# Kernel tuning notes

Measured on AMD Instinct MI355X. Metric: run time of the kernel, lower is better.

## Reference

```python
import jax, jax.numpy as jnp
import numpy as np

N = 4096
D_FEAT = 64


def setup_inputs() -> dict:
    key = jax.random.key(0)
    kx, ky = jax.random.split(key)
    xINP = jax.random.normal(kx, (N, D_FEAT), dtype=jnp.float32)
    yINP = jax.random.normal(ky, (N, D_FEAT), dtype=jnp.float32)
    return {"xINP": xINP, "yINP": yINP}


def _greedy_match(xINP, yINP):
    n = xINP.shape[0]
    # Euclidean (p=2) distance matrix, same as scipy.spatial.distance_matrix
    x2 = jnp.sum(xINP * xINP, axis=1)[:, None]           # [n, 1]
    y2 = jnp.sum(yINP * yINP, axis=1)[None, :]           # [1, n]
    sq = jnp.maximum(x2 + y2 - 2.0 * (xINP @ yINP.T), 0.0)
    cost = jnp.sqrt(sq)                                   # [n, n]
    # sorted() with key is stable; jnp.argsort is stable by default
    order = jnp.argsort(cost.reshape(-1))                 # [n*n]

    row0 = jnp.full((n,), -1, dtype=jnp.int32)
    col0 = jnp.full((n,), -1, dtype=jnp.int32)

    def body(k, state):
        row, col = state
        idx = order[k]
        i = idx // n
        j = idx % n
        free = (row[i] == -1) & (col[j] == -1)
        row = row.at[i].set(jnp.where(free, j.astype(jnp.int32), row[i]))
        col = col.at[j].set(jnp.where(free, i.astype(jnp.int32), col[j]))
        return (row, col)

    row, _col = jax.lax.fori_loop(0, n * n, body, (row0, col0))
    return row  # row_to_col_match_vec, int32 in [-1, n)


def reference(xINP, yINP):
    return _greedy_match(xINP, yINP)
```

## Files before the change

### kernel.cpp

```cpp
#include <hip/hip_runtime.h>

#define N 4096
#define D 64
#define TCAP 1024
#define TTHRESH 96
#define SNB 256
#define SNT 512
#define S0B 1024
#define S0T 512
#define RPAIRS 14

typedef unsigned long long u64;

__device__ float g_C[(size_t)N * (size_t)N];
__device__ float g_tailC[(size_t)TCAP * TCAP];
__device__ float4 g_yT[N * 16];
__device__ float g_x2[N], g_y2[N];
__device__ int   g_rowMatch[N];
__device__ int   g_freeRows[2][N];
__device__ int   g_freeCols[2][N];
__device__ u64   g_rowMinR[2][N];
__device__ u64   g_colMin[2][N];
__device__ int   g_nr[2], g_nc[2];
__device__ int   g_done, g_finalCur;

__device__ inline u64 shfl_down_u64(u64 v, int d) {
  unsigned lo = (unsigned)(v & 0xffffffffull);
  unsigned hi = (unsigned)(v >> 32);
  lo = __shfl_down(lo, d, 64);
  hi = __shfl_down(hi, d, 64);
  return ((u64)hi << 32) | (u64)lo;
}

__device__ inline void block_rowmin_reduce8(u64* best, int rows, u64* s_part) {
  const int tid = threadIdx.x;
  const int lane = tid & 63;
  const int wv = tid >> 6;
#pragma unroll
  for (int r = 0; r < 16; ++r) {
    if (r < rows) {
      u64 v = best[r];
#pragma unroll
      for (int d = 32; d > 0; d >>= 1) {
        u64 o = shfl_down_u64(v, d);
        v = (o < v) ? o : v;
      }
      if (lane == 0) s_part[r * 8 + wv] = v;
    }
  }
  __syncthreads();
  if (tid < rows) {
    u64 mn = s_part[tid * 8];
#pragma unroll
    for (int w = 1; w < 8; ++w) {
      u64 o = s_part[tid * 8 + w];
      mn = (o < mn) ? o : mn;
    }
    s_part[128 + tid] = mn;
  }
}

__device__ __forceinline__ float f4e(const float4* a, int e) {
  float4 v = a[e >> 2];
  switch (e & 3) {
    case 0: return v.x;
    case 1: return v.y;
    case 2: return v.z;
    default: return v.w;
  }
}

__global__ void __launch_bounds__(256) k_init(const float* __restrict__ x,
                                              const float* __restrict__ y) {
  const int i = blockIdx.x * 256 + threadIdx.x;
  const float4* xr4 = reinterpret_cast<const float4*>(x + (size_t)i * D);
  const float4* yr4 = reinterpret_cast<const float4*>(y + (size_t)i * D);

  {
    float4 xv[16];
#pragma unroll
    for (int k = 0; k < 16; ++k) xv[k] = xr4[k];
    float qx[8];
#pragma unroll
    for (int j = 0; j < 8; ++j) {
      float v = f4e(xv, j);
      qx[j] = __fmul_rn(v, v);
    }
#pragma unroll
    for (int m = 8; m < D; m += 8) {
#pragma unroll
      for (int j = 0; j < 8; ++j) {
        float v = f4e(xv, m + j);
        qx[j] = __fadd_rn(qx[j], __fmul_rn(v, v));
      }
    }
    g_x2[i] = __fadd_rn(__fadd_rn(__fadd_rn(qx[0], qx[1]), __fadd_rn(qx[2], qx[3])),
                        __fadd_rn(__fadd_rn(qx[4], qx[5]), __fadd_rn(qx[6], qx[7])));
  }
  {
    float4 yv[16];
#pragma unroll
    for (int k = 0; k < 16; ++k) yv[k] = yr4[k];
    float qy[8];
#pragma unroll
    for (int j = 0; j < 8; ++j) {
      float w = f4e(yv, j);
      qy[j] = __fmul_rn(w, w);
    }
#pragma unroll
    for (int m = 8; m < D; m += 8) {
#pragma unroll
      for (int j = 0; j < 8; ++j) {
        float w = f4e(yv, m + j);
        qy[j] = __fadd_rn(qy[j], __fmul_rn(w, w));
      }
    }
    g_y2[i] = __fadd_rn(__fadd_rn(__fadd_rn(qy[0], qy[1]), __fadd_rn(qy[2], qy[3])),
                        __fadd_rn(__fadd_rn(qy[4], qy[5]), __fadd_rn(qy[6], qy[7])));
#pragma unroll
    for (int k = 0; k < 16; ++k) g_yT[(k << 12) + i] = yv[k];
  }

  g_rowMatch[i] = -1;
  g_freeRows[0][i] = i;
  g_freeCols[0][i] = i;
  g_rowMinR[0][i] = ~0ull;
  g_rowMinR[1][i] = ~0ull;
  g_colMin[0][i] = ~0ull;
  g_colMin[1][i] = ~0ull;
  if (i == 0) {
    g_nr[0] = N; g_nc[0] = N; g_nr[1] = 0; g_nc[1] = 0;
    g_done = 0;
    g_finalCur = ((RPAIRS & 1) ^ 1);
  }
}

__global__ void __launch_bounds__(S0T) k_scan0(const float* __restrict__ x,
                                               const float* __restrict__ y) {
  __shared__ u64 s_part[64 + 8];
  const int tid = threadIdx.x;
  const int r0 = (blockIdx.x >> 1) << 3;
  const int h = blockIdx.x & 1;

  float x2r[8];
#pragma unroll
  for (int r = 0; r < 8; ++r) x2r[r] = g_x2[r0 + r];
  u64 best[8];
#pragma unroll
  for (int r = 0; r < 8; ++r) best[r] = ~0ull;

  const int c0 = tid + (h << 11);
  float acc[8][4];
#pragma unroll
  for (int r = 0; r < 8; ++r)
#pragma unroll
    for (int k = 0; k < 4; ++k) acc[r][k] = 0.0f;

#pragma unroll
  for (int kc = 0; kc < 16; ++kc) {
    const float4* ytk = g_yT + (kc << 12);
    float4 yv0 = ytk[c0];
    float4 yv1 = ytk[c0 + 512];
    float4 yv2 = ytk[c0 + 1024];
    float4 yv3 = ytk[c0 + 1536];
#pragma unroll
    for (int r = 0; r < 8; ++r) {
      float4 xv = reinterpret_cast<const float4*>(x + (size_t)(r0 + r) * D)[kc];
      acc[r][0] = fmaf(xv.x, yv0.x, acc[r][0]);
      acc[r][0] = fmaf(xv.y, yv0.y, acc[r][0]);
      acc[r][0] = fmaf(xv.z, yv0.z, acc[r][0]);
      acc[r][0] = fmaf(xv.w, yv0.w, acc[r][0]);
      acc[r][1] = fmaf(xv.x, yv1.x, acc[r][1]);
      acc[r][1] = fmaf(xv.y, yv1.y, acc[r][1]);
      acc[r][1] = fmaf(xv.z, yv1.z, acc[r][1]);
      acc[r][1] = fmaf(xv.w, yv1.w, acc[r][1]);
      acc[r][2] = fmaf(xv.x, yv2.x, acc[r][2]);
      acc[r][2] = fmaf(xv.y, yv2.y, acc[r][2]);
      acc[r][2] = fmaf(xv.z, yv2.z, acc[r][2]);
      acc[r][2] = fmaf(xv.w, yv2.w, acc[r][2]);
      acc[r][3] = fmaf(xv.x, yv3.x, acc[r][3]);
      acc[r][3] = fmaf(xv.y, yv3.y, acc[r][3]);
      acc[r][3] = fmaf(xv.z, yv3.z, acc[r][3]);
      acc[r][3] = fmaf(xv.w, yv3.w, acc[r][3]);
    }
  }

#pragma unroll
  for (int k = 0; k < 4; ++k) {
    const int c = c0 + (k << 9);
    const float y2j = g_y2[c];
    u64 ckey = ~0ull;
#pragma unroll
    for (int r = 0; r < 8; ++r) {
      float t = __fadd_rn(x2r[r], y2j);
      float sq = __fsub_rn(t, __fmul_rn(2.0f, acc[r][k]));
      sq = fmaxf(sq, 0.0f);
      float cost = __fsqrt_rn(sq);
      g_C[(size_t)(r0 + r) * N + c] = cost;
      u64 cb = ((u64)__float_as_uint(cost)) << 32;
      u64 rk = cb | (unsigned)c;
      best[r] = (rk < best[r]) ? rk : best[r];
      u64 ck = cb | (unsigned)(r0 + r);
      ckey = (ck < ckey) ? ck : ckey;
    }
    u64 curv = g_colMin[0][c];
    if (ckey < curv) atomicMin((unsigned long long*)&g_colMin[0][c], ckey);
  }

  {
    const int lane = tid & 63, wv = tid >> 6;
#pragma unroll
    for (int r = 0; r < 8; ++r) {
      u64 v = best[r];
#pragma unroll
      for (int d = 32; d > 0; d >>= 1) {
        u64 o = shfl_down_u64(v, d);
        v = (o < v) ? o : v;
      }
      if (lane == 0) s_part[r * 8 + wv] = v;
    }
    __syncthreads();
    if (tid < 8) {
      u64 mn = s_part[tid * 8];
#pragma unroll
      for (int w = 1; w < 8; ++w) {
        u64 o = s_part[tid * 8 + w];
        mn = (o < mn) ? o : mn;
      }
      u64 curv = g_rowMinR[0][r0 + tid];
      if (mn < curv) atomicMin((unsigned long long*)&g_rowMinR[0][r0 + tid], mn);
    }
  }
  (void)y;
}

__global__ void __launch_bounds__(SNT, 2) k_scanN(int round) {
  if (g_done) return;
  const int cur = round & 1;
  const int nr = g_nr[cur], nc = g_nc[cur];
  const int tid = threadIdx.x, bid = blockIdx.x;

  for (int t = bid * SNT + tid; t < N; t += SNB * SNT) {
    g_colMin[cur ^ 1][t] = ~0ull;
    g_rowMinR[cur ^ 1][t] = ~0ull;
  }

  const int ngroups = (nr + 15) >> 4;
  int lgS = 0;
  while (lgS < 4 && (ngroups << (lgS + 1)) <= SNB) ++lgS;
  const int S = 1 << lgS;
  if (bid >= (ngroups << lgS)) return;
  const int g = bid >> lgS;
  const int s = bid & (S - 1);

  __shared__ u64 s_colPart[4096];
  __shared__ u64 s_part[128 + 16];
  __shared__ int s_irow[16];

  const int r0 = g << 4;
  const int rows = min(16, nr - r0);
  if (tid < 16) {
    int rr = (tid < rows) ? (r0 + tid) : r0;
    s_irow[tid] = g_freeRows[cur][rr];
  }
  const int cstart = (s << 9) + tid;
  const int cstep = S << 9;
  for (int c = cstart; c < nc; c += cstep) s_colPart[c] = ~0ull;
  __syncthreads();

  int ir[16];
#pragma unroll
  for (int r = 0; r < 16; ++r) ir[r] = s_irow[r];
  u64 best[16];
#pragma unroll
  for (int r = 0; r < 16; ++r) best[r] = ~0ull;

  for (int c = cstart; c < nc; c += cstep) {
    const int j = g_freeCols[cur][c];
    u64 cpart = s_colPart[c];
#pragma unroll
    for (int r = 0; r < 16; ++r) {
      if (r < rows) {
        float cost = g_C[(size_t)ir[r] * N + j];
        u64 cb = ((u64)__float_as_uint(cost)) << 32;
        u64 rk = cb | (unsigned)j;
        best[r] = (rk < best[r]) ? rk : best[r];
        u64 ck = cb | (unsigned)ir[r];
        cpart = (ck < cpart) ? ck : cpart;
      }
    }
    s_colPart[c] = cpart;
  }

  block_rowmin_reduce8(best, rows, s_part);
  if (tid < rows) {
    u64 k = s_part[128 + tid];
    u64 curv = g_rowMinR[cur][s_irow[tid]];
    if (k < curv) atomicMin((unsigned long long*)&g_rowMinR[cur][s_irow[tid]], k);
  }

  for (int c = cstart; c < nc; c += cstep) {
    u64 k = s_colPart[c];
    if (k != ~0ull) {
      int j = g_freeCols[cur][c];
      u64 curv = g_colMin[cur][j];
      if (k < curv) atomicMin((unsigned long long*)&g_colMin[cur][j], k);
    }
  }
}

__global__ void __launch_bounds__(SNT) k_match(int round) {
  if (g_done) return;
  const int cur = round & 1, nxt = cur ^ 1;
  const int tid = threadIdx.x, bid = blockIdx.x;
  const int nr = g_nr[cur], nc = g_nc[cur];
  __shared__ int s_wc[8];
  __shared__ int s_base;

  const int lane = tid & 63, wv = tid >> 6;
  if (bid == 0) {
    if (tid == 0) s_base = 0;
    __syncthreads();
    for (int start = 0; start < nr; start += SNT) {
      int r = start + tid;
      int keep = 0; int iv = -1;
      if (r < nr) {
        int i = g_freeRows[cur][r];
        iv = i;
        int j = (int)(unsigned)(g_rowMinR[cur][i] & 0xffffffffull);
        u64 cm = g_colMin[cur][j];
        if ((int)(unsigned)(cm & 0xffffffffull) == i) g_rowMatch[i] = j;
        else keep = 1;
      }
      u64 bm = __ballot(keep);
      int pre = __popcll(bm & ((1ull << lane) - 1ull));
      if (lane == 0) s_wc[wv] = __popcll(bm);
      __syncthreads();
      int off = 0, tot = 0;
#pragma unroll
      for (int w = 0; w < 8; ++w) { off += (w < wv) ? s_wc[w] : 0; tot += s_wc[w]; }
      if (keep) g_freeRows[nxt][s_base + off + pre] = iv;
      __syncthreads();
      if (tid == 0) s_base += tot;
      __syncthreads();
    }
    if (tid == 0) {
      int nnr = s_base;
      g_nr[nxt] = nnr;
      if (nnr <= TTHRESH || nnr >= nr) { g_finalCur = nxt; g_done = 1; }
    }
  } else {
    if (tid == 0) s_base = 0;
    __syncthreads();
    for (int start = 0; start < nc; start += SNT) {
      int c = start + tid;
      int keep = 0; int jv = -1;
      if (c < nc) {
        int j = g_freeCols[cur][c];
        jv = j;
        u64 cm = g_colMin[cur][j];
        int i2 = (int)(unsigned)(cm & 0xffffffffull);
        int bj = (int)(unsigned)(g_rowMinR[cur][i2] & 0xffffffffull);
        if (bj != j) keep = 1;
      }
      u64 bm = __ballot(keep);
      int pre = __popcll(bm & ((1ull << lane) - 1ull));
      if (lane == 0) s_wc[wv] = __popcll(bm);
      __syncthreads();
      int off = 0, tot = 0;
#pragma unroll
      for (int w = 0; w < 8; ++w) { off += (w < wv) ? s_wc[w] : 0; tot += s_wc[w]; }
      if (keep) g_freeCols[nxt][s_base + off + pre] = jv;
      __syncthreads();
      if (tid == 0) s_base += tot;
      __syncthreads();
    }
    if (tid == 0) g_nc[nxt] = s_base;
  }
}

__global__ void __launch_bounds__(SNT) k_gather() {
  const int fc = g_finalCur;
  const int mr = g_nr[fc], mc = g_nc[fc];
  if (mr <= 0 || mr > TCAP || mc <= 0 || mc > TCAP) return;
  const int tid = threadIdx.x, bid = blockIdx.x;
  for (int rr = bid; rr < mr; rr += SNB) {
    const int irow = g_freeRows[fc][rr];
    const float* src = g_C + (size_t)irow * N;
    float* dst = g_tailC + (size_t)rr * TCAP;
    for (int c = tid; c < mc; c += SNT) {
      dst[c] = src[g_freeCols[fc][c]];
    }
  }
}

__global__ void __launch_bounds__(1024, 1) k_tail(int* __restrict__ out) {
  __shared__ int s_rpos[2][TCAP], s_cpos[2][TCAP];
  __shared__ int s_rbest[TCAP];
  __shared__ u64 s_cmin[TCAP];
  __shared__ int s_wc[16];
  const int tid = threadIdx.x;
  const int lane = tid & 63, wv = tid >> 6;

  const int fc = g_finalCur;
  int mr = g_nr[fc], mc = g_nc[fc];
  if (mr < 0 || mr > TCAP || mc < 0 || mc > TCAP) mr = 0;
  for (int t = tid; t < mr; t += 1024) s_rpos[0][t] = t;
  for (int t = tid; t < mc; t += 1024) s_cpos[0][t] = t;
  __syncthreads();

  int tcur = 0;
  for (int round = 0; round < 2048 && mr > 0; ++round) {
    const int nit = (mc + 63) >> 6;
    int cpv[16];
#pragma unroll
    for (int k = 0; k < 16; ++k) {
      int ci = (k << 6) + lane;
      cpv[k] = (k < nit && ci < mc) ? s_cpos[tcur][ci] : 0;
    }
    for (int rr = wv; rr < mr; rr += 16) {
      const int rp = s_rpos[tcur][rr];
      const float* rowp = g_tailC + (size_t)rp * TCAP;
      u64 best = ~0ull;
#pragma unroll
      for (int k = 0; k < 16; ++k) {
        if (k < nit) {
          int ci = (k << 6) + lane;
          if (ci < mc) {
            float cost = rowp[cpv[k]];
            u64 key = (((u64)__float_as_uint(cost)) << 32) | (unsigned)ci;
            best = (key < best) ? key : best;
          }
        }
      }
#pragma unroll
      for (int d = 32; d > 0; d >>= 1) {
        u64 o = shfl_down_u64(best, d);
        best = (o < best) ? o : best;
      }
      if (lane == 0) s_rbest[rr] = (int)(best & 0xffffffffull);
    }
    __syncthreads();
    if (tid < mc) {
      const int cp = s_cpos[tcur][tid];
      const float* colp = g_tailC + cp;
      u64 best = ~0ull;
      int r = 0;
      for (; r + 4 <= mr; r += 4) {
#pragma unroll
        for (int q = 0; q < 4; ++q) {
          int rp = s_rpos[tcur][r + q];
          float cost = colp[(size_t)rp * TCAP];
          u64 key = (((u64)__float_as_uint(cost)) << 32) | (unsigned)(r + q);
          best = (key < best) ? key : best;
        }
      }
      for (; r < mr; ++r) {
        int rp = s_rpos[tcur][r];
        float cost = colp[(size_t)rp * TCAP];
        u64 key = (((u64)__float_as_uint(cost)) << 32) | (unsigned)r;
        best = (key < best) ? key : best;
      }
      s_cmin[tid] = best;
    }
    __syncthreads();
    int keep = 0;
    if (tid < mr) {
      int q = s_rbest[tid];
      if ((int)(unsigned)(s_cmin[q] & 0xffffffffull) == tid) {
        g_rowMatch[g_freeRows[fc][s_rpos[tcur][tid]]] = g_freeCols[fc][s_cpos[tcur][q]];
      } else keep = 1;
    }
    u64 bm = __ballot(keep);
    int pre = __popcll(bm & ((1ull << lane) - 1ull));
    if (lane == 0) s_wc[wv] = __popcll(bm);
    __syncthreads();
    int off = 0, tot = 0;
#pragma unroll
    for (int w = 0; w < 16; ++w) { off += (w < wv) ? s_wc[w] : 0; tot += s_wc[w]; }
    if (keep) s_rpos[tcur ^ 1][off + pre] = s_rpos[tcur][tid];
    int newmr = tot;
    __syncthreads();
    int keepc = 0;
    if (tid < mc) {
      int r2 = (int)(unsigned)(s_cmin[tid] & 0xffffffffull);
      if (s_rbest[r2] != tid) keepc = 1;
    }
    u64 bm2 = __ballot(keepc);
    int pre2 = __popcll(bm2 & ((1ull << lane) - 1ull));
    if (lane == 0) s_wc[wv] = __popcll(bm2);
    __syncthreads();
    int off2 = 0, tot2 = 0;
#pragma unroll
    for (int w = 0; w < 16; ++w) { off2 += (w < wv) ? s_wc[w] : 0; tot2 += s_wc[w]; }
    if (keepc) s_cpos[tcur ^ 1][off2 + pre2] = s_cpos[tcur][tid];
    __syncthreads();
    if (newmr >= mr) break;
    mr = newmr; mc = tot2; tcur ^= 1;
  }
  __syncthreads();
  for (int i = tid; i < N; i += 1024) out[i] = g_rowMatch[i];
}

extern "C" void kernel_launch(void* const* d_in, const int* in_sizes, int n_in,
                              void* d_out, int out_size, void* d_ws, size_t ws_size,
                              hipStream_t stream) {
  const float* x = (const float*)d_in[0];
  const float* y = (const float*)d_in[1];
  int* out = (int*)d_out;
  k_init<<<16, 256, 0, stream>>>(x, y);
  k_scan0<<<S0B, S0T, 0, stream>>>(x, y);
  k_match<<<2, SNT, 0, stream>>>(0);
  for (int r = 1; r <= RPAIRS; ++r) {
    k_scanN<<<SNB, SNT, 0, stream>>>(r);
    k_match<<<2, SNT, 0, stream>>>(r);
  }
  k_gather<<<SNB, SNT, 0, stream>>>();
  k_tail<<<1, 1024, 0, stream>>>(out);
  (void)in_sizes; (void)n_in; (void)out_size; (void)d_ws; (void)ws_size;
}
```

Before: 787.7 us.

## Track top-2 row/col minima to match more pairs per round

The scan kernel now keeps the two smallest keys per free row and per free column, and merges them with paired atomicMin inserts. The match kernel uses these second minima to resolve a second tier of mutual-best pairs: a pair whose first choice was taken by another mutual match can still be committed in the same round. The aim is to shrink the free set faster so fewer scan/match rounds are needed, and RPAIRS drops from 14 to 9 to match. In exchange each scan pass costs more (extra shared memory, registers, compares and atomics), and the second-tier logic may not exactly reproduce the greedy order.

```diff
diff --git a/kernel.cpp b/kernel.cpp
--- a/kernel.cpp
+++ b/kernel.cpp
@@ -8,9 +8,10 @@
 #define SNT 512
 #define S0B 1024
 #define S0T 512
-#define RPAIRS 14
+#define RPAIRS 9
 
 typedef unsigned long long u64;
+#define LO32(k) ((int)(unsigned)((k) & 0xffffffffull))
 
 __device__ float g_C[(size_t)N * (size_t)N];
 __device__ float g_tailC[(size_t)TCAP * TCAP];
@@ -20,7 +21,9 @@
 __device__ int   g_freeRows[2][N];
 __device__ int   g_freeCols[2][N];
 __device__ u64   g_rowMinR[2][N];
+__device__ u64   g_rowMin2[2][N];
 __device__ u64   g_colMin[2][N];
+__device__ u64   g_colMin2[2][N];
 __device__ int   g_nr[2], g_nc[2];
 __device__ int   g_done, g_finalCur;
 
@@ -70,6 +73,13 @@
   }
 }
 
+__device__ __forceinline__ void insert2(u64* m1, u64* m2, u64 k) {
+  if (k == ~0ull) return;
+  u64 old = atomicMin((unsigned long long*)m1, k);
+  u64 loser = (k < old) ? old : k;
+  if (loser != ~0ull) atomicMin((unsigned long long*)m2, loser);
+}
+
 __global__ void __launch_bounds__(256) k_init(const float* __restrict__ x,
                                               const float* __restrict__ y) {
   const int i = blockIdx.x * 256 + threadIdx.x;
@@ -126,8 +136,12 @@
   g_freeCols[0][i] = i;
   g_rowMinR[0][i] = ~0ull;
   g_rowMinR[1][i] = ~0ull;
+  g_rowMin2[0][i] = ~0ull;
+  g_rowMin2[1][i] = ~0ull;
   g_colMin[0][i] = ~0ull;
   g_colMin[1][i] = ~0ull;
+  g_colMin2[0][i] = ~0ull;
+  g_colMin2[1][i] = ~0ull;
   if (i == 0) {
     g_nr[0] = N; g_nc[0] = N; g_nr[1] = 0; g_nc[1] = 0;
     g_done = 0;
@@ -242,7 +256,9 @@
 
   for (int t = bid * SNT + tid; t < N; t += SNB * SNT) {
     g_colMin[cur ^ 1][t] = ~0ull;
+    g_colMin2[cur ^ 1][t] = ~0ull;
     g_rowMinR[cur ^ 1][t] = ~0ull;
+    g_rowMin2[cur ^ 1][t] = ~0ull;
   }
 
   const int ngroups = (nr + 15) >> 4;
@@ -253,8 +269,10 @@
   const int g = bid >> lgS;
   const int s = bid & (S - 1);
 
-  __shared__ u64 s_colPart[4096];
-  __shared__ u64 s_part[128 + 16];
+  __shared__ u64 s_cp1[4096];
+  __shared__ u64 s_cp2[4096];
+  __shared__ u64 s_p1[128 + 16];
+  __shared__ u64 s_p2[128 + 16];
   __shared__ int s_irow[16];
 
   const int r0 = g << 4;
@@ -265,46 +283,78 @@
   }
   const int cstart = (s << 9) + tid;
   const int cstep = S << 9;
-  for (int c = cstart; c < nc; c += cstep) s_colPart[c] = ~0ull;
+  for (int c = cstart; c < nc; c += cstep) { s_cp1[c] = ~0ull; s_cp2[c] = ~0ull; }
   __syncthreads();
 
   int ir[16];
 #pragma unroll
   for (int r = 0; r < 16; ++r) ir[r] = s_irow[r];
-  u64 best[16];
-#pragma unroll
-  for (int r = 0; r < 16; ++r) best[r] = ~0ull;
+  u64 b1[16], b2[16];
+#pragma unroll
+  for (int r = 0; r < 16; ++r) { b1[r] = ~0ull; b2[r] = ~0ull; }
 
   for (int c = cstart; c < nc; c += cstep) {
     const int j = g_freeCols[cur][c];
-    u64 cpart = s_colPart[c];
+    u64 c1 = s_cp1[c], c2 = s_cp2[c];
 #pragma unroll
     for (int r = 0; r < 16; ++r) {
       if (r < rows) {
         float cost = g_C[(size_t)ir[r] * N + j];
         u64 cb = ((u64)__float_as_uint(cost)) << 32;
         u64 rk = cb | (unsigned)j;
-        best[r] = (rk < best[r]) ? rk : best[r];
+        if (rk < b1[r]) { b2[r] = b1[r]; b1[r] = rk; }
+        else if (rk < b2[r]) b2[r] = rk;
         u64 ck = cb | (unsigned)ir[r];
-        cpart = (ck < cpart) ? ck : cpart;
-      }
-    }
-    s_colPart[c] = cpart;
-  }
-
-  block_rowmin_reduce8(best, rows, s_part);
-  if (tid < rows) {
-    u64 k = s_part[128 + tid];
-    u64 curv = g_rowMinR[cur][s_irow[tid]];
-    if (k < curv) atomicMin((unsigned long long*)&g_rowMinR[cur][s_irow[tid]], k);
+        if (ck < c1) { c2 = c1; c1 = ck; }
+        else if (ck < c2) c2 = ck;
+      }
+    }
+    s_cp1[c] = c1; s_cp2[c] = c2;
+  }
+
+  {
+    const int lane = tid & 63, wv = tid >> 6;
+#pragma unroll
+    for (int r = 0; r < 16; ++r) {
+      if (r < rows) {
+        u64 v1 = b1[r], v2 = b2[r];
+#pragma unroll
+        for (int d = 32; d > 0; d >>= 1) {
+          u64 o1 = shfl_down_u64(v1, d);
+          u64 o2 = shfl_down_u64(v2, d);
+          u64 n1 = (v1 < o1) ? v1 : o1;
+          u64 hi = (v1 < o1) ? o1 : v1;
+          u64 lo = (v2 < o2) ? v2 : o2;
+          v1 = n1;
+          v2 = (hi < lo) ? hi : lo;
+        }
+        if (lane == 0) { s_p1[r * 8 + wv] = v1; s_p2[r * 8 + wv] = v2; }
+      }
+    }
+    __syncthreads();
+    if (tid < rows) {
+      u64 m1 = s_p1[tid * 8], m2 = s_p2[tid * 8];
+#pragma unroll
+      for (int w = 1; w < 8; ++w) {
+        u64 o1 = s_p1[tid * 8 + w], o2 = s_p2[tid * 8 + w];
+        u64 n1 = (m1 < o1) ? m1 : o1;
+        u64 hi = (m1 < o1) ? o1 : m1;
+        u64 lo = (m2 < o2) ? m2 : o2;
+        m1 = n1;
+        m2 = (hi < lo) ? hi : lo;
+      }
+      const int i = s_irow[tid];
+      insert2(&g_rowMinR[cur][i], &g_rowMin2[cur][i], m1);
+      insert2(&g_rowMinR[cur][i], &g_rowMin2[cur][i], m2);
+    }
   }
 
   for (int c = cstart; c < nc; c += cstep) {
-    u64 k = s_colPart[c];
-    if (k != ~0ull) {
-      int j = g_freeCols[cur][c];
-      u64 curv = g_colMin[cur][j];
-      if (k < curv) atomicMin((unsigned long long*)&g_colMin[cur][j], k);
+    u64 k1 = s_cp1[c];
+    if (k1 != ~0ull) {
+      const int j = g_freeCols[cur][c];
+      insert2(&g_colMin[cur][j], &g_colMin2[cur][j], k1);
+      insert2(&g_colMin[cur][j], &g_colMin2[cur][j], s_cp2[c]);
     }
   }
 }
@@ -327,10 +377,41 @@
       if (r < nr) {
         int i = g_freeRows[cur][r];
         iv = i;
-        int j = (int)(unsigned)(g_rowMinR[cur][i] & 0xffffffffull);
-        u64 cm = g_colMin[cur][j];
-        if ((int)(unsigned)(cm & 0xffffffffull) == i) g_rowMatch[i] = j;
-        else keep = 1;
+        u64 rm1 = g_rowMinR[cur][i];
+        int j1 = LO32(rm1);
+        int i1 = LO32(g_colMin[cur][j1]);
+        if (i1 == i) {
+          g_rowMatch[i] = j1;
+        } else {
+          int jc = -1;
+          bool j1gone = (LO32(g_rowMinR[cur][i1]) == j1);
+          if (!j1gone) jc = j1;
+          else {
+            u64 rm2 = g_rowMin2[cur][i];
+            if (rm2 != ~0ull) {
+              int j2 = LO32(rm2);
+              int i2 = LO32(g_colMin[cur][j2]);
+              if (LO32(g_rowMinR[cur][i2]) != j2) jc = j2;
+            }
+          }
+          int rc = -1;
+          if (jc >= 0) {
+            int r1 = LO32(g_colMin[cur][jc]);
+            int jr1 = LO32(g_rowMinR[cur][r1]);
+            bool r1m = (LO32(g_colMin[cur][jr1]) == r1);
+            if (!r1m) rc = r1;
+            else {
+              u64 cm2 = g_colMin2[cur][jc];
+              if (cm2 != ~0ull) {
+                int r2 = LO32(cm2);
+                int jr2 = LO32(g_rowMinR[cur][r2]);
+                if (LO32(g_colMin[cur][jr2]) != r2) rc = r2;
+              }
+            }
+          }
+          if (jc >= 0 && rc == i) g_rowMatch[i] = jc;
+          else keep = 1;
+        }
       }
       u64 bm = __ballot(keep);
       int pre = __popcll(bm & ((1ull << lane) - 1ull));
@@ -358,10 +439,42 @@
       if (c < nc) {
         int j = g_freeCols[cur][c];
         jv = j;
-        u64 cm = g_colMin[cur][j];
-        int i2 = (int)(unsigned)(cm & 0xffffffffull);
-        int bj = (int)(unsigned)(g_rowMinR[cur][i2] & 0xffffffffull);
-        if (bj != j) keep = 1;
+        u64 cm1 = g_colMin[cur][j];
+        int i1 = LO32(cm1);
+        if (LO32(g_rowMinR[cur][i1]) == j) {
+        } else {
+          int rc = -1;
+          {
+            int r1 = i1;
+            int jr1 = LO32(g_rowMinR[cur][r1]);
+            bool r1m = (LO32(g_colMin[cur][jr1]) == r1);
+            if (!r1m) rc = r1;
+            else {
+              u64 cm2 = g_colMin2[cur][j];
+              if (cm2 != ~0ull) {
+                int r2 = LO32(cm2);
+                int jr2 = LO32(g_rowMinR[cur][r2]);
+                if (LO32(g_colMin[cur][jr2]) != r2) rc = r2;
+              }
+            }
+          }
+          int jc = -1;
+          if (rc >= 0) {
+            int jA = LO32(g_rowMinR[cur][rc]);
+            int iA = LO32(g_colMin[cur][jA]);
+            bool jAgone = (LO32(g_rowMinR[cur][iA]) == jA);
+            if (!jAgone) jc = jA;
+            else {
+              u64 rm2 = g_rowMin2[cur][rc];
+              if (rm2 != ~0ull) {
+                int jB = LO32(rm2);
+                int iB = LO32(g_colMin[cur][jB]);
+                if (LO32(g_rowMinR[cur][iB]) != jB) jc = jB;
+              }
+            }
+          }
+          if (!(rc >= 0 && jc == j)) keep = 1;
+        }
       }
       u64 bm = __ballot(keep);
       int pre = __popcll(bm & ((1ull << lane) - 1ull));
```

Result: faster. 709.1 us (-10.0%).
